# Optimization experiments

Hardware: AMD Instinct MI355X
Metric: run time of the kernel (lower is better)

Reference implementation:

```python
import jax, jax.numpy as jnp
import numpy as np

EPS = 1e-5

def layer_norm(x, g, b):
    m = x.mean(-1, keepdims=True)
    v = ((x - m) ** 2).mean(-1, keepdims=True)
    return (x - m) * jax.lax.rsqrt(v + EPS) * g + b

def setup_inputs() -> dict:
    key = jax.random.key(0)
    ks = jax.random.split(key, 12)
    H = 2048; E = 2048; I = 2048; N = 32
    A = (H + E) // 2  # attention hidden = 2048
    s = lambda fan: 1.0 / np.sqrt(fan)
    inp = {
        "input":   jax.random.normal(ks[0], (I,), jnp.float32),
        "hiddens": jax.random.normal(ks[1], (N, H), jnp.float32),
        "cells":   jax.random.normal(ks[2], (N, H), jnp.float32),
        "external":jax.random.normal(ks[3], (E,), jnp.float32),
        # weights (torch nn.Linear layout: [out, in]); LN enabled -> no biases on linears
        "W_ai":   jax.random.uniform(ks[4], (A, H + E), jnp.float32, -s(H+E), s(H+E)),
        "W_attn": jax.random.uniform(ks[5], (1, A), jnp.float32, -s(A), s(A)),
        "W_merge":jax.random.uniform(ks[6], (H, H), jnp.float32, -s(H), s(H)),
        "W_iou":  jax.random.uniform(ks[7], (3 * H, I + H), jnp.float32, -s(I+H), s(I+H)),
        "W_fi":   jax.random.uniform(ks[8], (H, I), jnp.float32, -s(I), s(I)),
        "W_fh":   jax.random.uniform(ks[9], (H, H), jnp.float32, -s(H), s(H)),
        "g_merge": jnp.ones((H,), jnp.float32), "b_merge": jnp.zeros((H,), jnp.float32),
        "g_f": jnp.ones((H,), jnp.float32), "b_f": jnp.zeros((H,), jnp.float32),
        "g_i": jnp.ones((H,), jnp.float32), "b_i": jnp.zeros((H,), jnp.float32),
        "g_o": jnp.ones((H,), jnp.float32), "b_o": jnp.zeros((H,), jnp.float32),
        "g_u": jnp.ones((H,), jnp.float32), "b_u": jnp.zeros((H,), jnp.float32),
        "g_c": jnp.ones((H,), jnp.float32), "b_c": jnp.zeros((H,), jnp.float32),
    }
    return inp

def reference(input, hiddens, cells, external,
              W_ai, W_attn, W_merge, W_iou, W_fi, W_fh,
              g_merge, b_merge, g_f, b_f, g_i, b_i, g_o, b_o, g_u, b_u, g_c, b_c):
    N, H = hiddens.shape
    # forget-gate preactivations: [H] + [N,H] -> [N,H]
    f_lin = input @ W_fi.T + hiddens @ W_fh.T
    # attentive merge over children
    ext = jnp.broadcast_to(external, (N, external.shape[0]))
    ai = jnp.tanh(jnp.concatenate([hiddens, ext], axis=1) @ W_ai.T)       # [N, (H+E)//2]
    attn = jax.nn.softmax(ai @ W_attn.T, axis=0)                          # [N, 1]
    merged = (hiddens * attn).sum(0)                                      # [H]
    merge_hidden = jnp.tanh(layer_norm(merged @ W_merge.T, g_merge, b_merge))
    # i/o/u gates from [input ; merged_hidden]
    iou = jnp.concatenate([input, merge_hidden]) @ W_iou.T                # [3H]
    i_l, o_l, u_l = jnp.split(iou, 3)
    f = jax.nn.sigmoid(layer_norm(f_lin, g_f, b_f))                       # [N,H]
    i = jax.nn.sigmoid(layer_norm(i_l, g_i, b_i))
    o = jax.nn.sigmoid(layer_norm(o_l, g_o, b_o))
    u = jnp.tanh(layer_norm(u_l, g_u, b_u))                               # dropout=0 -> identity
    new_cell = layer_norm(i * u + (f * cells).sum(0), g_c, b_c)           # [H]
    new_h = o * jnp.tanh(new_cell)
    return new_h, new_cell
```

## Files before the change

kernel.cpp:

```cpp
#include <hip/hip_runtime.h>
#include <hip/hip_bf16.h>

typedef __bf16 bf16_t;
typedef __attribute__((ext_vector_type(8))) __bf16 bf16x8;
typedef __attribute__((ext_vector_type(4))) float f32x4;

#define EPSF 1e-5f

__global__ __launch_bounds__(256) void s1_mega(
    const float* __restrict__ hiddens, const float* __restrict__ external,
    const float* __restrict__ input,
    const float* __restrict__ W_ai, const float* __restrict__ W_fh,
    const float* __restrict__ W_fi, const float* __restrict__ W_attn,
    float* __restrict__ lp, float* __restrict__ fh_out, float* __restrict__ fi_out)
{
    __shared__ float red[4][2][16][16];
    __shared__ float ejs[4][16];

    int b    = blockIdx.x;
    int tid  = threadIdx.x;
    int wave = tid >> 6;
    int lane = tid & 63;

    if (b < 256) {
        bool is_ai = (b < 128);
        int  jt    = is_ai ? b : b - 128;
        int  l15   = lane & 15;
        int  quad  = lane >> 4;
        int  k0    = wave * 512;
        int  wstride = is_ai ? 4096 : 2048;
        const float* W = is_ai ? W_ai : W_fh;

        const float* a0p = hiddens + (size_t)l15 * 2048 + quad * 8 + k0;
        const float* a1p = hiddens + (size_t)(16 + l15) * 2048 + quad * 8 + k0;
        const float* bp  = W + (size_t)(jt * 16 + l15) * wstride + quad * 8 + k0;

        f32x4 acc0 = {0.f, 0.f, 0.f, 0.f};
        f32x4 acc1 = {0.f, 0.f, 0.f, 0.f};
        float ejacc = 0.f;

        if (is_ai) {
            const float* ep = bp + 2048;
            const float* xp = external + quad * 8 + k0;
            #pragma unroll 2
            for (int k = 0; k < 512; k += 32) {
                float4 p0 = *(const float4*)(a0p + k);
                float4 p1 = *(const float4*)(a0p + k + 4);
                float4 q0 = *(const float4*)(a1p + k);
                float4 q1 = *(const float4*)(a1p + k + 4);
                float4 b0 = *(const float4*)(bp + k);
                float4 b1 = *(const float4*)(bp + k + 4);
                float4 e0 = *(const float4*)(ep + k);
                float4 e1 = *(const float4*)(ep + k + 4);
                float4 x0 = *(const float4*)(xp + k);
                float4 x1 = *(const float4*)(xp + k + 4);
                bf16x8 av0, av1, bv;
                av0[0]=(bf16_t)p0.x; av0[1]=(bf16_t)p0.y; av0[2]=(bf16_t)p0.z; av0[3]=(bf16_t)p0.w;
                av0[4]=(bf16_t)p1.x; av0[5]=(bf16_t)p1.y; av0[6]=(bf16_t)p1.z; av0[7]=(bf16_t)p1.w;
                av1[0]=(bf16_t)q0.x; av1[1]=(bf16_t)q0.y; av1[2]=(bf16_t)q0.z; av1[3]=(bf16_t)q0.w;
                av1[4]=(bf16_t)q1.x; av1[5]=(bf16_t)q1.y; av1[6]=(bf16_t)q1.z; av1[7]=(bf16_t)q1.w;
                bv[0]=(bf16_t)b0.x; bv[1]=(bf16_t)b0.y; bv[2]=(bf16_t)b0.z; bv[3]=(bf16_t)b0.w;
                bv[4]=(bf16_t)b1.x; bv[5]=(bf16_t)b1.y; bv[6]=(bf16_t)b1.z; bv[7]=(bf16_t)b1.w;
                acc0 = __builtin_amdgcn_mfma_f32_16x16x32_bf16(av0, bv, acc0, 0, 0, 0);
                acc1 = __builtin_amdgcn_mfma_f32_16x16x32_bf16(av1, bv, acc1, 0, 0, 0);
                ejacc += e0.x*x0.x + e0.y*x0.y + e0.z*x0.z + e0.w*x0.w
                       + e1.x*x1.x + e1.y*x1.y + e1.z*x1.z + e1.w*x1.w;
            }
            ejacc += __shfl_xor(ejacc, 16, 64);
            ejacc += __shfl_xor(ejacc, 32, 64);
            if (quad == 0) ejs[wave][l15] = ejacc;
        } else {
            #pragma unroll 2
            for (int k = 0; k < 512; k += 32) {
                float4 p0 = *(const float4*)(a0p + k);
                float4 p1 = *(const float4*)(a0p + k + 4);
                float4 q0 = *(const float4*)(a1p + k);
                float4 q1 = *(const float4*)(a1p + k + 4);
                float4 b0 = *(const float4*)(bp + k);
                float4 b1 = *(const float4*)(bp + k + 4);
                bf16x8 av0, av1, bv;
                av0[0]=(bf16_t)p0.x; av0[1]=(bf16_t)p0.y; av0[2]=(bf16_t)p0.z; av0[3]=(bf16_t)p0.w;
                av0[4]=(bf16_t)p1.x; av0[5]=(bf16_t)p1.y; av0[6]=(bf16_t)p1.z; av0[7]=(bf16_t)p1.w;
                av1[0]=(bf16_t)q0.x; av1[1]=(bf16_t)q0.y; av1[2]=(bf16_t)q0.z; av1[3]=(bf16_t)q0.w;
                av1[4]=(bf16_t)q1.x; av1[5]=(bf16_t)q1.y; av1[6]=(bf16_t)q1.z; av1[7]=(bf16_t)q1.w;
                bv[0]=(bf16_t)b0.x; bv[1]=(bf16_t)b0.y; bv[2]=(bf16_t)b0.z; bv[3]=(bf16_t)b0.w;
                bv[4]=(bf16_t)b1.x; bv[5]=(bf16_t)b1.y; bv[6]=(bf16_t)b1.z; bv[7]=(bf16_t)b1.w;
                acc0 = __builtin_amdgcn_mfma_f32_16x16x32_bf16(av0, bv, acc0, 0, 0, 0);
                acc1 = __builtin_amdgcn_mfma_f32_16x16x32_bf16(av1, bv, acc1, 0, 0, 0);
            }
        }

        #pragma unroll
        for (int r = 0; r < 4; ++r) {
            red[wave][0][quad * 4 + r][l15] = acc0[r];
            red[wave][1][quad * 4 + r][l15] = acc1[r];
        }
        __syncthreads();

        int row = tid >> 4, col = tid & 15;
        #pragma unroll
        for (int nt = 0; nt < 2; ++nt) {
            float s = red[0][nt][row][col] + red[1][nt][row][col]
                    + red[2][nt][row][col] + red[3][nt][row][col];
            if (is_ai) {
                float ej = ejs[0][col] + ejs[1][col] + ejs[2][col] + ejs[3][col];
                float lg = tanhf(s + ej) * W_attn[jt * 16 + col];
                lg += __shfl_xor(lg, 1, 64);
                lg += __shfl_xor(lg, 2, 64);
                lg += __shfl_xor(lg, 4, 64);
                lg += __shfl_xor(lg, 8, 64);
                if (col == 0) lp[jt * 32 + nt * 16 + row] = lg;
            } else {
                fh_out[(size_t)(nt * 16 + row) * 2048 + jt * 16 + col] = s;
            }
        }
    } else {
        int nb = b - 256;
        int base, nr;
        if (nb < 128) { base = nb * 4;              nr = 1; }
        else          { base = 512 + (nb - 128) * 12; nr = 3; }
        for (int r = 0; r < nr; ++r) {
            int row = base + wave * nr + r;
            const float4* wp = (const float4*)(W_fi + (size_t)row * 2048) + lane;
            const float4* xp = (const float4*)input + lane;
            float acc2 = 0.f;
            #pragma unroll
            for (int k = 0; k < 512; k += 64) {
                float4 w = wp[k];
                float4 v = xp[k];
                acc2 += w.x*v.x + w.y*v.y + w.z*v.z + w.w*v.w;
            }
            #pragma unroll
            for (int off = 32; off; off >>= 1) acc2 += __shfl_down(acc2, off, 64);
            if (lane == 0) fi_out[row] = acc2;
        }
    }
}

__global__ __launch_bounds__(256) void s2_mega(
    const float* __restrict__ fi, const float* __restrict__ fh,
    const float* __restrict__ lp, const float* __restrict__ hiddens,
    float* __restrict__ frs, float* __restrict__ merged)
{
    __shared__ float s1[256], s2[256];
    int b = blockIdx.x, t = threadIdx.x;

    if (b < 32) {
        int n = b;
        float sum = 0.f, sq = 0.f;
        #pragma unroll
        for (int i = 0; i < 8; ++i) {
            int h = t * 8 + i;
            float v = fi[h] + fh[n * 2048 + h];
            sum += v; sq += v * v;
        }
        s1[t] = sum; s2[t] = sq;
        __syncthreads();
        for (int off = 128; off; off >>= 1) {
            if (t < off) { s1[t] += s1[t + off]; s2[t] += s2[t + off]; }
            __syncthreads();
        }
        if (t == 0) {
            const float inv = 1.f / 2048.f;
            float mean = s1[0] * inv;
            frs[n * 2]     = mean;
            frs[n * 2 + 1] = rsqrtf(s2[0] * inv - mean * mean + EPSF);
        }
    } else {
        __shared__ float lred[32][8];
        __shared__ float attnw[32];
        int n = t >> 3, sl = t & 7;
        float p = 0.f;
        #pragma unroll
        for (int m = 0; m < 16; ++m) p += lp[(sl * 16 + m) * 32 + n];
        lred[n][sl] = p;
        __syncthreads();
        if (sl == 0) {
            float lg = 0.f;
            #pragma unroll
            for (int m = 0; m < 8; ++m) lg += lred[n][m];
            lred[n][0] = lg;
        }
        __syncthreads();
        if (t < 32) {
            float mx = -1e30f;
            for (int m = 0; m < 32; ++m) mx = fmaxf(mx, lred[m][0]);
            float ssum = 0.f;
            for (int m = 0; m < 32; ++m) ssum += expf(lred[m][0] - mx);
            attnw[t] = expf(lred[t][0] - mx) / ssum;
        }
        __syncthreads();
        int h = (b - 32) * 256 + t;
        float acc = 0.f;
        #pragma unroll 8
        for (int n2 = 0; n2 < 32; ++n2) acc += attnw[n2] * hiddens[n2 * 2048 + h];
        merged[h] = acc;
    }
}

__global__ __launch_bounds__(256) void s3_mega(
    const float* __restrict__ W_merge, const float* __restrict__ merged,
    const float* __restrict__ fi, const float* __restrict__ fh,
    const float* __restrict__ frs, const float* __restrict__ gf,
    const float* __restrict__ bf_, const float* __restrict__ cells,
    float* __restrict__ mm, float* __restrict__ fc)
{
    int b = blockIdx.x, t = threadIdx.x;
    if (b < 512) {
        int row  = b * 4 + (t >> 6);
        int lane = t & 63;
        const float4* wp = (const float4*)(W_merge + (size_t)row * 2048) + lane;
        const float4* xp = (const float4*)merged + lane;
        float acc = 0.f;
        #pragma unroll
        for (int k = 0; k < 512; k += 64) {
            float4 w = wp[k];
            float4 v = xp[k];
            acc += w.x*v.x + w.y*v.y + w.z*v.z + w.w*v.w;
        }
        #pragma unroll
        for (int off = 32; off; off >>= 1) acc += __shfl_down(acc, off, 64);
        if (lane == 0) mm[row] = acc;
    } else {
        int h = (b - 512) * 256 + t;
        float g = gf[h], bb = bf_[h], f_i = fi[h];
        float acc = 0.f;
        for (int n = 0; n < 32; ++n) {
            float v = (f_i + fh[n * 2048 + h] - frs[n * 2]) * frs[n * 2 + 1] * g + bb;
            float f = 1.f / (1.f + expf(-v));
            acc += f * cells[n * 2048 + h];
        }
        fc[h] = acc;
    }
}

__global__ __launch_bounds__(256, 3) void s4_iou(
    const float* __restrict__ W_iou, const float* __restrict__ mm,
    const float* __restrict__ input, const float* __restrict__ g,
    const float* __restrict__ bvec, float* __restrict__ iou)
{
    int b = blockIdx.x, t = threadIdx.x;
    int wave = t >> 6, lane = t & 63;

    const float4* mm4 = (const float4*)mm;
    const float4* in4 = (const float4*)input;
    const float4* g4  = (const float4*)g;
    const float4* b4  = (const float4*)bvec;

    float4 mv[8];
    #pragma unroll
    for (int k = 0; k < 8; ++k) mv[k] = mm4[lane + 64 * k];
    float sum = 0.f, sq = 0.f;
    #pragma unroll
    for (int k = 0; k < 8; ++k) {
        sum += mv[k].x + mv[k].y + mv[k].z + mv[k].w;
        sq  += mv[k].x*mv[k].x + mv[k].y*mv[k].y + mv[k].z*mv[k].z + mv[k].w*mv[k].w;
    }
    #pragma unroll
    for (int off = 1; off < 64; off <<= 1) {
        sum += __shfl_xor(sum, off, 64);
        sq  += __shfl_xor(sq,  off, 64);
    }
    const float inv = 1.f / 2048.f;
    float mean = sum * inv;
    float r = rsqrtf(sq * inv - mean * mean + EPSF);

    float4 xr[16];
    #pragma unroll
    for (int k = 0; k < 8; ++k) xr[k] = in4[lane + 64 * k];
    #pragma unroll
    for (int k = 0; k < 8; ++k) {
        float4 gv = g4[lane + 64 * k];
        float4 bv = b4[lane + 64 * k];
        xr[8 + k].x = tanhf((mv[k].x - mean) * r * gv.x + bv.x);
        xr[8 + k].y = tanhf((mv[k].y - mean) * r * gv.y + bv.y);
        xr[8 + k].z = tanhf((mv[k].z - mean) * r * gv.z + bv.z);
        xr[8 + k].w = tanhf((mv[k].w - mean) * r * gv.w + bv.w);
    }

    int row0 = (b * 4 + wave) * 2;
    for (int rr = 0; rr < 2; ++rr) {
        const float4* wp = (const float4*)(W_iou + (size_t)(row0 + rr) * 4096);
        float acc = 0.f;
        #pragma unroll
        for (int k = 0; k < 16; ++k) {
            float4 w = wp[lane + 64 * k];
            acc += w.x*xr[k].x + w.y*xr[k].y + w.z*xr[k].z + w.w*xr[k].w;
        }
        #pragma unroll
        for (int off = 32; off; off >>= 1) acc += __shfl_down(acc, off, 64);
        if (lane == 0) iou[row0 + rr] = acc;
    }
}

__global__ __launch_bounds__(256) void s5_tail(
    const float* __restrict__ iou, const float* __restrict__ fc,
    const float* __restrict__ gi, const float* __restrict__ bi,
    const float* __restrict__ go, const float* __restrict__ bo,
    const float* __restrict__ gu, const float* __restrict__ bu,
    const float* __restrict__ gc, const float* __restrict__ bc,
    float* __restrict__ out)
{
    __shared__ float sA[6][256];
    int t = threadIdx.x;
    float vi[8], vo[8], vu[8];
    float si = 0, qi = 0, so = 0, qo = 0, su = 0, qu = 0;
    #pragma unroll
    for (int i = 0; i < 8; ++i) {
        int h = t * 8 + i;
        vi[i] = iou[h]; vo[i] = iou[2048 + h]; vu[i] = iou[4096 + h];
        si += vi[i]; qi += vi[i] * vi[i];
        so += vo[i]; qo += vo[i] * vo[i];
        su += vu[i]; qu += vu[i] * vu[i];
    }
    sA[0][t] = si; sA[1][t] = qi; sA[2][t] = so;
    sA[3][t] = qo; sA[4][t] = su; sA[5][t] = qu;
    __syncthreads();
    for (int off = 128; off; off >>= 1) {
        if (t < off) {
            #pragma unroll
            for (int c = 0; c < 6; ++c) sA[c][t] += sA[c][t + off];
        }
        __syncthreads();
    }
    const float inv = 1.f / 2048.f;
    float mi = sA[0][0] * inv, ri = rsqrtf(sA[1][0] * inv - mi * mi + EPSF);
    float mo = sA[2][0] * inv, ro = rsqrtf(sA[3][0] * inv - mo * mo + EPSF);
    float mu = sA[4][0] * inv, ru = rsqrtf(sA[5][0] * inv - mu * mu + EPSF);
    __syncthreads();

    float o_[8], v_[8];
    float sv = 0, qv = 0;
    #pragma unroll
    for (int i = 0; i < 8; ++i) {
        int h = t * 8 + i;
        float ivl = 1.f / (1.f + expf(-((vi[i] - mi) * ri * gi[h] + bi[h])));
        o_[i]     = 1.f / (1.f + expf(-((vo[i] - mo) * ro * go[h] + bo[h])));
        float uvl = tanhf((vu[i] - mu) * ru * gu[h] + bu[h]);
        v_[i] = ivl * uvl + fc[h];
        sv += v_[i]; qv += v_[i] * v_[i];
    }
    sA[0][t] = sv; sA[1][t] = qv;
    __syncthreads();
    for (int off = 128; off; off >>= 1) {
        if (t < off) { sA[0][t] += sA[0][t + off]; sA[1][t] += sA[1][t + off]; }
        __syncthreads();
    }
    float mc = sA[0][0] * inv, rc = rsqrtf(sA[1][0] * inv - mc * mc + EPSF);
    #pragma unroll
    for (int i = 0; i < 8; ++i) {
        int h = t * 8 + i;
        float nc = (v_[i] - mc) * rc * gc[h] + bc[h];
        float nh = o_[i] * tanhf(nc);
        out[h]        = nh;
        out[2048 + h] = nc;
    }
}

extern "C" void kernel_launch(void* const* d_in, const int* in_sizes, int n_in,
                              void* d_out, int out_size, void* d_ws, size_t ws_size,
                              hipStream_t stream)
{
    const float* input    = (const float*)d_in[0];
    const float* hiddens  = (const float*)d_in[1];
    const float* cells    = (const float*)d_in[2];
    const float* external = (const float*)d_in[3];
    const float* W_ai     = (const float*)d_in[4];
    const float* W_attn   = (const float*)d_in[5];
    const float* W_merge  = (const float*)d_in[6];
    const float* W_iou    = (const float*)d_in[7];
    const float* W_fi     = (const float*)d_in[8];
    const float* W_fh     = (const float*)d_in[9];
    const float* g_merge  = (const float*)d_in[10];
    const float* b_merge  = (const float*)d_in[11];
    const float* g_f      = (const float*)d_in[12];
    const float* b_f      = (const float*)d_in[13];
    const float* g_i      = (const float*)d_in[14];
    const float* b_i      = (const float*)d_in[15];
    const float* g_o      = (const float*)d_in[16];
    const float* b_o      = (const float*)d_in[17];
    const float* g_u      = (const float*)d_in[18];
    const float* b_u      = (const float*)d_in[19];
    const float* g_c      = (const float*)d_in[20];
    const float* b_c      = (const float*)d_in[21];

    float* ws = (float*)d_ws;
    float* ws_fh     = ws;
    float* ws_fi     = ws + 65536;
    float* ws_lp     = ws + 67584;
    float* ws_frs    = ws + 71680;
    float* ws_merged = ws + 71744;
    float* ws_mm     = ws + 73792;
    float* ws_fc     = ws + 75840;
    float* ws_iou    = ws + 77888;
    float* out = (float*)d_out;

    s1_mega<<<512, 256, 0, stream>>>(hiddens, external, input,
                                     W_ai, W_fh, W_fi, W_attn,
                                     ws_lp, ws_fh, ws_fi);
    s2_mega<<<40, 256, 0, stream>>>(ws_fi, ws_fh, ws_lp, hiddens,
                                    ws_frs, ws_merged);
    s3_mega<<<520, 256, 0, stream>>>(W_merge, ws_merged, ws_fi, ws_fh,
                                     ws_frs, g_f, b_f, cells, ws_mm, ws_fc);
    s4_iou<<<768, 256, 0, stream>>>(W_iou, ws_mm, input, g_merge, b_merge, ws_iou);
    s5_tail<<<1, 256, 0, stream>>>(ws_iou, ws_fc, g_i, b_i, g_o, b_o,
                                   g_u, b_u, g_c, b_c, out);
}
```

Measured before the change: 281.4 us.

## Fuse five stage kernels into one persistent kernel with grid barriers

Replaces the five kernel launches with a single 256-block persistent kernel that separates the stages with atomic-counter grid barriers. The input half of the W_iou GEMV is moved into stage 1 so it can run early, and stage 4 accumulates the merged-hidden half into the same buffer. This targets the launch gaps and tail idling between dependent small stages. In exchange it depends on all 256 blocks being co-resident, adds a memset and spin-wait cost, and removes the unroll pragmas from the MFMA loops.

```diff
diff --git a/kernel.cpp b/kernel.cpp
--- a/kernel.cpp
+++ b/kernel.cpp
@@ -6,23 +6,49 @@
 typedef __attribute__((ext_vector_type(4))) float f32x4;
 
 #define EPSF 1e-5f
-
-__global__ __launch_bounds__(256) void s1_mega(
-    const float* __restrict__ hiddens, const float* __restrict__ external,
-    const float* __restrict__ input,
-    const float* __restrict__ W_ai, const float* __restrict__ W_fh,
-    const float* __restrict__ W_fi, const float* __restrict__ W_attn,
-    float* __restrict__ lp, float* __restrict__ fh_out, float* __restrict__ fi_out)
+#define NB 256
+
+__device__ __forceinline__ void gbar(int* cnt, int target) {
+    __syncthreads();
+    if (threadIdx.x == 0) {
+        __hip_atomic_fetch_add(cnt, 1, __ATOMIC_ACQ_REL, __HIP_MEMORY_SCOPE_AGENT);
+        while (__hip_atomic_load(cnt, __ATOMIC_ACQUIRE, __HIP_MEMORY_SCOPE_AGENT) < target)
+            __builtin_amdgcn_s_sleep(2);
+    }
+    __syncthreads();
+}
+
+__global__ __launch_bounds__(256, 2) void fused_cell(
+    const float* __restrict__ input, const float* __restrict__ hiddens,
+    const float* __restrict__ cells, const float* __restrict__ external,
+    const float* __restrict__ W_ai, const float* __restrict__ W_attn,
+    const float* __restrict__ W_merge, const float* __restrict__ W_iou,
+    const float* __restrict__ W_fi, const float* __restrict__ W_fh,
+    const float* __restrict__ g_merge, const float* __restrict__ b_merge,
+    const float* __restrict__ g_f, const float* __restrict__ b_f,
+    const float* __restrict__ gi, const float* __restrict__ bi,
+    const float* __restrict__ go, const float* __restrict__ bo,
+    const float* __restrict__ gu, const float* __restrict__ bu,
+    const float* __restrict__ gc, const float* __restrict__ bc,
+    float* __restrict__ ws_fh, float* __restrict__ ws_fi,
+    float* __restrict__ ws_lp, float* __restrict__ ws_frs,
+    float* __restrict__ ws_merged, float* __restrict__ ws_mm,
+    float* __restrict__ ws_fc, float* __restrict__ ws_iou,
+    int* __restrict__ bar, float* __restrict__ out)
 {
     __shared__ float red[4][2][16][16];
     __shared__ float ejs[4][16];
+    __shared__ float sb1[256], sb2[256];
+    __shared__ float lred[32][8];
+    __shared__ float attnw[32];
+    __shared__ float sA6[6][256];
 
     int b    = blockIdx.x;
     int tid  = threadIdx.x;
     int wave = tid >> 6;
     int lane = tid & 63;
 
-    if (b < 256) {
+    {
         bool is_ai = (b < 128);
         int  jt    = is_ai ? b : b - 128;
         int  l15   = lane & 15;
@@ -42,7 +68,6 @@
         if (is_ai) {
             const float* ep = bp + 2048;
             const float* xp = external + quad * 8 + k0;
-            #pragma unroll 2
             for (int k = 0; k < 512; k += 32) {
                 float4 p0 = *(const float4*)(a0p + k);
                 float4 p1 = *(const float4*)(a0p + k + 4);
@@ -70,7 +95,6 @@
             ejacc += __shfl_xor(ejacc, 32, 64);
             if (quad == 0) ejs[wave][l15] = ejacc;
         } else {
-            #pragma unroll 2
             for (int k = 0; k < 512; k += 32) {
                 float4 p0 = *(const float4*)(a0p + k);
                 float4 p1 = *(const float4*)(a0p + k + 4);
@@ -109,70 +133,68 @@
                 lg += __shfl_xor(lg, 2, 64);
                 lg += __shfl_xor(lg, 4, 64);
                 lg += __shfl_xor(lg, 8, 64);
-                if (col == 0) lp[jt * 32 + nt * 16 + row] = lg;
+                if (col == 0) ws_lp[jt * 32 + nt * 16 + row] = lg;
             } else {
-                fh_out[(size_t)(nt * 16 + row) * 2048 + jt * 16 + col] = s;
-            }
-        }
-    } else {
-        int nb = b - 256;
-        int base, nr;
-        if (nb < 128) { base = nb * 4;              nr = 1; }
-        else          { base = 512 + (nb - 128) * 12; nr = 3; }
-        for (int r = 0; r < nr; ++r) {
-            int row = base + wave * nr + r;
-            const float4* wp = (const float4*)(W_fi + (size_t)row * 2048) + lane;
-            const float4* xp = (const float4*)input + lane;
-            float acc2 = 0.f;
-            #pragma unroll
-            for (int k = 0; k < 512; k += 64) {
-                float4 w = wp[k];
-                float4 v = xp[k];
-                acc2 += w.x*v.x + w.y*v.y + w.z*v.z + w.w*v.w;
-            }
-            #pragma unroll
-            for (int off = 32; off; off >>= 1) acc2 += __shfl_down(acc2, off, 64);
-            if (lane == 0) fi_out[row] = acc2;
-        }
-    }
-}
-
-__global__ __launch_bounds__(256) void s2_mega(
-    const float* __restrict__ fi, const float* __restrict__ fh,
-    const float* __restrict__ lp, const float* __restrict__ hiddens,
-    float* __restrict__ frs, float* __restrict__ merged)
-{
-    __shared__ float s1[256], s2[256];
-    int b = blockIdx.x, t = threadIdx.x;
+                ws_fh[(size_t)(nt * 16 + row) * 2048 + jt * 16 + col] = s;
+            }
+        }
+
+        const float4* in4 = (const float4*)input;
+        float4 xr[8];
+        #pragma unroll
+        for (int k = 0; k < 8; ++k) xr[k] = in4[lane + 64 * k];
+
+        int base  = is_ai ? jt * 24 : 3072 + jt * 40;
+        int nrows = is_ai ? 6 : 10;
+        int r0 = base + wave * nrows;
+        for (int i = 0; i < nrows; ++i) {
+            int r = r0 + i;
+            const float4* wp = (r < 2048)
+                ? (const float4*)(W_fi + (size_t)r * 2048)
+                : (const float4*)(W_iou + (size_t)(r - 2048) * 4096);
+            float acc = 0.f;
+            #pragma unroll
+            for (int k = 0; k < 8; ++k) {
+                float4 w = wp[lane + 64 * k];
+                acc += w.x*xr[k].x + w.y*xr[k].y + w.z*xr[k].z + w.w*xr[k].w;
+            }
+            #pragma unroll
+            for (int off = 32; off; off >>= 1) acc += __shfl_down(acc, off, 64);
+            if (lane == 0) {
+                if (r < 2048) ws_fi[r] = acc;
+                else          ws_iou[r - 2048] = acc;
+            }
+        }
+    }
+
+    gbar(bar, NB);
 
     if (b < 32) {
         int n = b;
         float sum = 0.f, sq = 0.f;
         #pragma unroll
         for (int i = 0; i < 8; ++i) {
-            int h = t * 8 + i;
-            float v = fi[h] + fh[n * 2048 + h];
+            int h = tid * 8 + i;
+            float v = ws_fi[h] + ws_fh[n * 2048 + h];
             sum += v; sq += v * v;
         }
-        s1[t] = sum; s2[t] = sq;
+        sb1[tid] = sum; sb2[tid] = sq;
         __syncthreads();
         for (int off = 128; off; off >>= 1) {
-            if (t < off) { s1[t] += s1[t + off]; s2[t] += s2[t + off]; }
+            if (tid < off) { sb1[tid] += sb1[tid + off]; sb2[tid] += sb2[tid + off]; }
             __syncthreads();
         }
-        if (t == 0) {
+        if (tid == 0) {
             const float inv = 1.f / 2048.f;
-            float mean = s1[0] * inv;
-            frs[n * 2]     = mean;
-            frs[n * 2 + 1] = rsqrtf(s2[0] * inv - mean * mean + EPSF);
-        }
-    } else {
-        __shared__ float lred[32][8];
-        __shared__ float attnw[32];
-        int n = t >> 3, sl = t & 7;
+            float mean = sb1[0] * inv;
+            ws_frs[n * 2]     = mean;
+            ws_frs[n * 2 + 1] = rsqrtf(sb2[0] * inv - mean * mean + EPSF);
+        }
+    } else if (b < 40) {
+        int n = tid >> 3, sl = tid & 7;
         float p = 0.f;
         #pragma unroll
-        for (int m = 0; m < 16; ++m) p += lp[(sl * 16 + m) * 32 + n];
+        for (int m = 0; m < 16; ++m) p += ws_lp[(sl * 16 + m) * 32 + n];
         lred[n][sl] = p;
         __syncthreads();
         if (sl == 0) {
@@ -182,178 +204,162 @@
             lred[n][0] = lg;
         }
         __syncthreads();
-        if (t < 32) {
+        if (tid < 32) {
             float mx = -1e30f;
             for (int m = 0; m < 32; ++m) mx = fmaxf(mx, lred[m][0]);
             float ssum = 0.f;
             for (int m = 0; m < 32; ++m) ssum += expf(lred[m][0] - mx);
-            attnw[t] = expf(lred[t][0] - mx) / ssum;
-        }
-        __syncthreads();
-        int h = (b - 32) * 256 + t;
+            attnw[tid] = expf(lred[tid][0] - mx) / ssum;
+        }
+        __syncthreads();
+        int h = (b - 32) * 256 + tid;
         float acc = 0.f;
         #pragma unroll 8
         for (int n2 = 0; n2 < 32; ++n2) acc += attnw[n2] * hiddens[n2 * 2048 + h];
-        merged[h] = acc;
-    }
-}
-
-__global__ __launch_bounds__(256) void s3_mega(
-    const float* __restrict__ W_merge, const float* __restrict__ merged,
-    const float* __restrict__ fi, const float* __restrict__ fh,
-    const float* __restrict__ frs, const float* __restrict__ gf,
-    const float* __restrict__ bf_, const float* __restrict__ cells,
-    float* __restrict__ mm, float* __restrict__ fc)
-{
-    int b = blockIdx.x, t = threadIdx.x;
-    if (b < 512) {
-        int row  = b * 4 + (t >> 6);
-        int lane = t & 63;
-        const float4* wp = (const float4*)(W_merge + (size_t)row * 2048) + lane;
-        const float4* xp = (const float4*)merged + lane;
-        float acc = 0.f;
-        #pragma unroll
-        for (int k = 0; k < 512; k += 64) {
-            float4 w = wp[k];
-            float4 v = xp[k];
-            acc += w.x*v.x + w.y*v.y + w.z*v.z + w.w*v.w;
-        }
-        #pragma unroll
-        for (int off = 32; off; off >>= 1) acc += __shfl_down(acc, off, 64);
-        if (lane == 0) mm[row] = acc;
-    } else {
-        int h = (b - 512) * 256 + t;
-        float g = gf[h], bb = bf_[h], f_i = fi[h];
-        float acc = 0.f;
-        for (int n = 0; n < 32; ++n) {
-            float v = (f_i + fh[n * 2048 + h] - frs[n * 2]) * frs[n * 2 + 1] * g + bb;
-            float f = 1.f / (1.f + expf(-v));
-            acc += f * cells[n * 2048 + h];
-        }
-        fc[h] = acc;
-    }
-}
-
-__global__ __launch_bounds__(256, 3) void s4_iou(
-    const float* __restrict__ W_iou, const float* __restrict__ mm,
-    const float* __restrict__ input, const float* __restrict__ g,
-    const float* __restrict__ bvec, float* __restrict__ iou)
-{
-    int b = blockIdx.x, t = threadIdx.x;
-    int wave = t >> 6, lane = t & 63;
-
-    const float4* mm4 = (const float4*)mm;
-    const float4* in4 = (const float4*)input;
-    const float4* g4  = (const float4*)g;
-    const float4* b4  = (const float4*)bvec;
-
-    float4 mv[8];
-    #pragma unroll
-    for (int k = 0; k < 8; ++k) mv[k] = mm4[lane + 64 * k];
-    float sum = 0.f, sq = 0.f;
-    #pragma unroll
-    for (int k = 0; k < 8; ++k) {
-        sum += mv[k].x + mv[k].y + mv[k].z + mv[k].w;
-        sq  += mv[k].x*mv[k].x + mv[k].y*mv[k].y + mv[k].z*mv[k].z + mv[k].w*mv[k].w;
-    }
-    #pragma unroll
-    for (int off = 1; off < 64; off <<= 1) {
-        sum += __shfl_xor(sum, off, 64);
-        sq  += __shfl_xor(sq,  off, 64);
-    }
-    const float inv = 1.f / 2048.f;
-    float mean = sum * inv;
-    float r = rsqrtf(sq * inv - mean * mean + EPSF);
-
-    float4 xr[16];
-    #pragma unroll
-    for (int k = 0; k < 8; ++k) xr[k] = in4[lane + 64 * k];
-    #pragma unroll
-    for (int k = 0; k < 8; ++k) {
-        float4 gv = g4[lane + 64 * k];
-        float4 bv = b4[lane + 64 * k];
-        xr[8 + k].x = tanhf((mv[k].x - mean) * r * gv.x + bv.x);
-        xr[8 + k].y = tanhf((mv[k].y - mean) * r * gv.y + bv.y);
-        xr[8 + k].z = tanhf((mv[k].z - mean) * r * gv.z + bv.z);
-        xr[8 + k].w = tanhf((mv[k].w - mean) * r * gv.w + bv.w);
-    }
-
-    int row0 = (b * 4 + wave) * 2;
-    for (int rr = 0; rr < 2; ++rr) {
-        const float4* wp = (const float4*)(W_iou + (size_t)(row0 + rr) * 4096);
-        float acc = 0.f;
-        #pragma unroll
-        for (int k = 0; k < 16; ++k) {
-            float4 w = wp[lane + 64 * k];
-            acc += w.x*xr[k].x + w.y*xr[k].y + w.z*xr[k].z + w.w*xr[k].w;
-        }
-        #pragma unroll
-        for (int off = 32; off; off >>= 1) acc += __shfl_down(acc, off, 64);
-        if (lane == 0) iou[row0 + rr] = acc;
-    }
-}
-
-__global__ __launch_bounds__(256) void s5_tail(
-    const float* __restrict__ iou, const float* __restrict__ fc,
-    const float* __restrict__ gi, const float* __restrict__ bi,
-    const float* __restrict__ go, const float* __restrict__ bo,
-    const float* __restrict__ gu, const float* __restrict__ bu,
-    const float* __restrict__ gc, const float* __restrict__ bc,
-    float* __restrict__ out)
-{
-    __shared__ float sA[6][256];
-    int t = threadIdx.x;
-    float vi[8], vo[8], vu[8];
-    float si = 0, qi = 0, so = 0, qo = 0, su = 0, qu = 0;
-    #pragma unroll
-    for (int i = 0; i < 8; ++i) {
-        int h = t * 8 + i;
-        vi[i] = iou[h]; vo[i] = iou[2048 + h]; vu[i] = iou[4096 + h];
-        si += vi[i]; qi += vi[i] * vi[i];
-        so += vo[i]; qo += vo[i] * vo[i];
-        su += vu[i]; qu += vu[i] * vu[i];
-    }
-    sA[0][t] = si; sA[1][t] = qi; sA[2][t] = so;
-    sA[3][t] = qo; sA[4][t] = su; sA[5][t] = qu;
-    __syncthreads();
-    for (int off = 128; off; off >>= 1) {
-        if (t < off) {
-            #pragma unroll
-            for (int c = 0; c < 6; ++c) sA[c][t] += sA[c][t + off];
-        }
-        __syncthreads();
-    }
-    const float inv = 1.f / 2048.f;
-    float mi = sA[0][0] * inv, ri = rsqrtf(sA[1][0] * inv - mi * mi + EPSF);
-    float mo = sA[2][0] * inv, ro = rsqrtf(sA[3][0] * inv - mo * mo + EPSF);
-    float mu = sA[4][0] * inv, ru = rsqrtf(sA[5][0] * inv - mu * mu + EPSF);
-    __syncthreads();
-
-    float o_[8], v_[8];
-    float sv = 0, qv = 0;
-    #pragma unroll
-    for (int i = 0; i < 8; ++i) {
-        int h = t * 8 + i;
-        float ivl = 1.f / (1.f + expf(-((vi[i] - mi) * ri * gi[h] + bi[h])));
-        o_[i]     = 1.f / (1.f + expf(-((vo[i] - mo) * ro * go[h] + bo[h])));
-        float uvl = tanhf((vu[i] - mu) * ru * gu[h] + bu[h]);
-        v_[i] = ivl * uvl + fc[h];
-        sv += v_[i]; qv += v_[i] * v_[i];
-    }
-    sA[0][t] = sv; sA[1][t] = qv;
-    __syncthreads();
-    for (int off = 128; off; off >>= 1) {
-        if (t < off) { sA[0][t] += sA[0][t + off]; sA[1][t] += sA[1][t + off]; }
-        __syncthreads();
-    }
-    float mc = sA[0][0] * inv, rc = rsqrtf(sA[1][0] * inv - mc * mc + EPSF);
-    #pragma unroll
-    for (int i = 0; i < 8; ++i) {
-        int h = t * 8 + i;
-        float nc = (v_[i] - mc) * rc * gc[h] + bc[h];
-        float nh = o_[i] * tanhf(nc);
-        out[h]        = nh;
-        out[2048 + h] = nc;
+        ws_merged[h] = acc;
+    }
+
+    gbar(bar, 2 * NB);
+
+    {
+        const float4* xp = (const float4*)ws_merged;
+        int rowc = b * 8 + wave * 2;
+        for (int rr = 0; rr < 2; ++rr) {
+            int row = rowc + rr;
+            const float4* wp = (const float4*)(W_merge + (size_t)row * 2048);
+            float acc = 0.f;
+            #pragma unroll
+            for (int k = 0; k < 8; ++k) {
+                float4 w = wp[lane + 64 * k];
+                float4 v = xp[lane + 64 * k];
+                acc += w.x*v.x + w.y*v.y + w.z*v.z + w.w*v.w;
+            }
+            #pragma unroll
+            for (int off = 32; off; off >>= 1) acc += __shfl_down(acc, off, 64);
+            if (lane == 0) ws_mm[row] = acc;
+        }
+        if (b < 8) {
+            int h = b * 256 + tid;
+            float g = g_f[h], bb = b_f[h], f_i = ws_fi[h];
+            float acc = 0.f;
+            for (int n = 0; n < 32; ++n) {
+                float v = (f_i + ws_fh[n * 2048 + h] - ws_frs[n * 2]) * ws_frs[n * 2 + 1] * g + bb;
+                float f = 1.f / (1.f + expf(-v));
+                acc += f * cells[n * 2048 + h];
+            }
+            ws_fc[h] = acc;
+        }
+    }
+
+    gbar(bar, 3 * NB);
+
+    {
+        const float4* mm4 = (const float4*)ws_mm;
+        const float4* g4  = (const float4*)g_merge;
+        const float4* b4  = (const float4*)b_merge;
+
+        float4 mv[8];
+        #pragma unroll
+        for (int k = 0; k < 8; ++k) mv[k] = mm4[lane + 64 * k];
+        float sum = 0.f, sq = 0.f;
+        #pragma unroll
+        for (int k = 0; k < 8; ++k) {
+            sum += mv[k].x + mv[k].y + mv[k].z + mv[k].w;
+            sq  += mv[k].x*mv[k].x + mv[k].y*mv[k].y + mv[k].z*mv[k].z + mv[k].w*mv[k].w;
+        }
+        #pragma unroll
+        for (int off = 1; off < 64; off <<= 1) {
+            sum += __shfl_xor(sum, off, 64);
+            sq  += __shfl_xor(sq,  off, 64);
+        }
+        const float inv = 1.f / 2048.f;
+        float mean = sum * inv;
+        float r = rsqrtf(sq * inv - mean * mean + EPSF);
+
+        float4 mh[8];
+        #pragma unroll
+        for (int k = 0; k < 8; ++k) {
+            float4 gv = g4[lane + 64 * k];
+            float4 bv = b4[lane + 64 * k];
+            mh[k].x = tanhf((mv[k].x - mean) * r * gv.x + bv.x);
+            mh[k].y = tanhf((mv[k].y - mean) * r * gv.y + bv.y);
+            mh[k].z = tanhf((mv[k].z - mean) * r * gv.z + bv.z);
+            mh[k].w = tanhf((mv[k].w - mean) * r * gv.w + bv.w);
+        }
+
+        int r0 = b * 24 + wave * 6;
+        for (int i = 0; i < 6; ++i) {
+            int row = r0 + i;
+            const float4* wp = (const float4*)(W_iou + (size_t)row * 4096 + 2048);
+            float acc = 0.f;
+            #pragma unroll
+            for (int k = 0; k < 8; ++k) {
+                float4 w = wp[lane + 64 * k];
+                acc += w.x*mh[k].x + w.y*mh[k].y + w.z*mh[k].z + w.w*mh[k].w;
+            }
+            #pragma unroll
+            for (int off = 32; off; off >>= 1) acc += __shfl_down(acc, off, 64);
+            if (lane == 0) ws_iou[row] += acc;
+        }
+    }
+
+    gbar(bar, 4 * NB);
+
+    if (b != 0) return;
+    {
+        int t = tid;
+        float vi[8], vo[8], vu[8];
+        float si = 0, qi = 0, so = 0, qo = 0, su = 0, qu = 0;
+        #pragma unroll
+        for (int i = 0; i < 8; ++i) {
+            int h = t * 8 + i;
+            vi[i] = ws_iou[h]; vo[i] = ws_iou[2048 + h]; vu[i] = ws_iou[4096 + h];
+            si += vi[i]; qi += vi[i] * vi[i];
+            so += vo[i]; qo += vo[i] * vo[i];
+            su += vu[i]; qu += vu[i] * vu[i];
+        }
+        sA6[0][t] = si; sA6[1][t] = qi; sA6[2][t] = so;
+        sA6[3][t] = qo; sA6[4][t] = su; sA6[5][t] = qu;
+        __syncthreads();
+        for (int off = 128; off; off >>= 1) {
+            if (t < off) {
+                #pragma unroll
+                for (int c = 0; c < 6; ++c) sA6[c][t] += sA6[c][t + off];
+            }
+            __syncthreads();
+        }
+        const float inv = 1.f / 2048.f;
+        float mi = sA6[0][0] * inv, ri = rsqrtf(sA6[1][0] * inv - mi * mi + EPSF);
+        float mo = sA6[2][0] * inv, ro = rsqrtf(sA6[3][0] * inv - mo * mo + EPSF);
+        float mu = sA6[4][0] * inv, ru = rsqrtf(sA6[5][0] * inv - mu * mu + EPSF);
+        __syncthreads();
+
+        float o_[8], v_[8];
+        float sv = 0, qv = 0;
+        #pragma unroll
+        for (int i = 0; i < 8; ++i) {
+            int h = t * 8 + i;
+            float ivl = 1.f / (1.f + expf(-((vi[i] - mi) * ri * gi[h] + bi[h])));
+            o_[i]     = 1.f / (1.f + expf(-((vo[i] - mo) * ro * go[h] + bo[h])));
+            float uvl = tanhf((vu[i] - mu) * ru * gu[h] + bu[h]);
+            v_[i] = ivl * uvl + ws_fc[h];
+            sv += v_[i]; qv += v_[i] * v_[i];
+        }
+        sA6[0][t] = sv; sA6[1][t] = qv;
+        __syncthreads();
+        for (int off = 128; off; off >>= 1) {
+            if (t < off) { sA6[0][t] += sA6[0][t + off]; sA6[1][t] += sA6[1][t + off]; }
+            __syncthreads();
+        }
+        float mc = sA6[0][0] * inv, rc = rsqrtf(sA6[1][0] * inv - mc * mc + EPSF);
+        #pragma unroll
+        for (int i = 0; i < 8; ++i) {
+            int h = t * 8 + i;
+            float nc = (v_[i] - mc) * rc * gc[h] + bc[h];
+            float nh = o_[i] * tanhf(nc);
+            out[h]        = nh;
+            out[2048 + h] = nc;
+        }
     }
 }
 
@@ -393,16 +399,14 @@
     float* ws_mm     = ws + 73792;
     float* ws_fc     = ws + 75840;
     float* ws_iou    = ws + 77888;
+    int*   ws_bar    = (int*)(ws + 84032);
     float* out = (float*)d_out;
 
-    s1_mega<<<512, 256, 0, stream>>>(hiddens, external, input,
-                                     W_ai, W_fh, W_fi, W_attn,
-                                     ws_lp, ws_fh, ws_fi);
-    s2_mega<<<40, 256, 0, stream>>>(ws_fi, ws_fh, ws_lp, hiddens,
-                                    ws_frs, ws_merged);
-    s3_mega<<<520, 256, 0, stream>>>(W_merge, ws_merged, ws_fi, ws_fh,
-                                     ws_frs, g_f, b_f, cells, ws_mm, ws_fc);
-    s4_iou<<<768, 256, 0, stream>>>(W_iou, ws_mm, input, g_merge, b_merge, ws_iou);
-    s5_tail<<<1, 256, 0, stream>>>(ws_iou, ws_fc, g_i, b_i, g_o, b_o,
-                                   g_u, b_u, g_c, b_c, out);
+    hipMemsetAsync(ws_bar, 0, 64, stream);
+    fused_cell<<<NB, 256, 0, stream>>>(input, hiddens, cells, external,
+                                       W_ai, W_attn, W_merge, W_iou, W_fi, W_fh,
+                                       g_merge, b_merge, g_f, b_f,
+                                       g_i, b_i, g_o, b_o, g_u, b_u, g_c, b_c,
+                                       ws_fh, ws_fi, ws_lp, ws_frs, ws_merged,
+                                       ws_mm, ws_fc, ws_iou, ws_bar, out);
 }
```

New measurement: 359.9 us. +27.9%, slower.

## Hoist input half of W_iou GEMV into first kernel and fuse tail via last-block

Applied to the files above, without the earlier changes.

The half of the iou GEMV that depends only on `input` (W_iou columns 0..2047) moves into the first kernel, where it streams alongside W_fi. Only the merge-dependent half is left on the critical path after W_merge. The separate single-block tail kernel is removed: the iou kernel uses an atomic done counter so the last block runs the final layer norms, saving a launch at the cost of a memset and fence/atomic overhead. Row indexing in k1 now covers 2048 fi rows plus 6144 iou rows over 512 extra blocks, each wave handling 4 rows with two rows loaded at once.

```diff
diff --git a/kernel.cpp b/kernel.cpp
--- a/kernel.cpp
+++ b/kernel.cpp
@@ -7,12 +7,14 @@
 
 #define EPSF 1e-5f
 
-__global__ __launch_bounds__(256) void s1_mega(
+__global__ __launch_bounds__(256, 3) void k1_streams(
     const float* __restrict__ hiddens, const float* __restrict__ external,
     const float* __restrict__ input,
     const float* __restrict__ W_ai, const float* __restrict__ W_fh,
-    const float* __restrict__ W_fi, const float* __restrict__ W_attn,
-    float* __restrict__ lp, float* __restrict__ fh_out, float* __restrict__ fi_out)
+    const float* __restrict__ W_fi, const float* __restrict__ W_iou,
+    const float* __restrict__ W_attn,
+    float* __restrict__ lp, float* __restrict__ fh_out,
+    float* __restrict__ fi_out, float* __restrict__ iou_out)
 {
     __shared__ float red[4][2][16][16];
     __shared__ float ejs[4][16];
@@ -115,29 +117,45 @@
             }
         }
     } else {
-        int nb = b - 256;
-        int base, nr;
-        if (nb < 128) { base = nb * 4;              nr = 1; }
-        else          { base = 512 + (nb - 128) * 12; nr = 3; }
-        for (int r = 0; r < nr; ++r) {
-            int row = base + wave * nr + r;
-            const float4* wp = (const float4*)(W_fi + (size_t)row * 2048) + lane;
-            const float4* xp = (const float4*)input + lane;
-            float acc2 = 0.f;
-            #pragma unroll
-            for (int k = 0; k < 512; k += 64) {
-                float4 w = wp[k];
-                float4 v = xp[k];
-                acc2 += w.x*v.x + w.y*v.y + w.z*v.z + w.w*v.w;
-            }
-            #pragma unroll
-            for (int off = 32; off; off >>= 1) acc2 += __shfl_down(acc2, off, 64);
-            if (lane == 0) fi_out[row] = acc2;
+        const float4* in4 = (const float4*)input;
+        float4 xr[8];
+        #pragma unroll
+        for (int k = 0; k < 8; ++k) xr[k] = in4[lane + 64 * k];
+
+        int r0 = (b - 256) * 16 + wave * 4;
+        #pragma unroll
+        for (int p = 0; p < 2; ++p) {
+            int ra = r0 + p * 2;
+            int rb = ra + 1;
+            const float4* wa = (ra < 2048)
+                ? (const float4*)(W_fi + (size_t)ra * 2048)
+                : (const float4*)(W_iou + (size_t)(ra - 2048) * 4096);
+            const float4* wb = (rb < 2048)
+                ? (const float4*)(W_fi + (size_t)rb * 2048)
+                : (const float4*)(W_iou + (size_t)(rb - 2048) * 4096);
+            float4 A[8], B[8];
+            #pragma unroll
+            for (int k = 0; k < 8; ++k) { A[k] = wa[lane + 64 * k]; B[k] = wb[lane + 64 * k]; }
+            float accA = 0.f, accB = 0.f;
+            #pragma unroll
+            for (int k = 0; k < 8; ++k) {
+                accA += A[k].x*xr[k].x + A[k].y*xr[k].y + A[k].z*xr[k].z + A[k].w*xr[k].w;
+                accB += B[k].x*xr[k].x + B[k].y*xr[k].y + B[k].z*xr[k].z + B[k].w*xr[k].w;
+            }
+            #pragma unroll
+            for (int off = 32; off; off >>= 1) {
+                accA += __shfl_down(accA, off, 64);
+                accB += __shfl_down(accB, off, 64);
+            }
+            if (lane == 0) {
+                if (ra < 2048) fi_out[ra] = accA; else iou_out[ra - 2048] = accA;
+                if (rb < 2048) fi_out[rb] = accB; else iou_out[rb - 2048] = accB;
+            }
         }
     }
 }
 
-__global__ __launch_bounds__(256) void s2_mega(
+__global__ __launch_bounds__(256) void k2_mid(
     const float* __restrict__ fi, const float* __restrict__ fh,
     const float* __restrict__ lp, const float* __restrict__ hiddens,
     float* __restrict__ frs, float* __restrict__ merged)
@@ -198,7 +216,7 @@
     }
 }
 
-__global__ __launch_bounds__(256) void s3_mega(
+__global__ __launch_bounds__(256) void k3_mid(
     const float* __restrict__ W_merge, const float* __restrict__ merged,
     const float* __restrict__ fi, const float* __restrict__ fh,
     const float* __restrict__ frs, const float* __restrict__ gf,
@@ -234,126 +252,135 @@
     }
 }
 
-__global__ __launch_bounds__(256, 3) void s4_iou(
+__global__ __launch_bounds__(256, 2) void k4_tail(
     const float* __restrict__ W_iou, const float* __restrict__ mm,
-    const float* __restrict__ input, const float* __restrict__ g,
-    const float* __restrict__ bvec, float* __restrict__ iou)
-{
-    int b = blockIdx.x, t = threadIdx.x;
-    int wave = t >> 6, lane = t & 63;
-
-    const float4* mm4 = (const float4*)mm;
-    const float4* in4 = (const float4*)input;
-    const float4* g4  = (const float4*)g;
-    const float4* b4  = (const float4*)bvec;
-
-    float4 mv[8];
-    #pragma unroll
-    for (int k = 0; k < 8; ++k) mv[k] = mm4[lane + 64 * k];
-    float sum = 0.f, sq = 0.f;
-    #pragma unroll
-    for (int k = 0; k < 8; ++k) {
-        sum += mv[k].x + mv[k].y + mv[k].z + mv[k].w;
-        sq  += mv[k].x*mv[k].x + mv[k].y*mv[k].y + mv[k].z*mv[k].z + mv[k].w*mv[k].w;
-    }
-    #pragma unroll
-    for (int off = 1; off < 64; off <<= 1) {
-        sum += __shfl_xor(sum, off, 64);
-        sq  += __shfl_xor(sq,  off, 64);
-    }
-    const float inv = 1.f / 2048.f;
-    float mean = sum * inv;
-    float r = rsqrtf(sq * inv - mean * mean + EPSF);
-
-    float4 xr[16];
-    #pragma unroll
-    for (int k = 0; k < 8; ++k) xr[k] = in4[lane + 64 * k];
-    #pragma unroll
-    for (int k = 0; k < 8; ++k) {
-        float4 gv = g4[lane + 64 * k];
-        float4 bv = b4[lane + 64 * k];
-        xr[8 + k].x = tanhf((mv[k].x - mean) * r * gv.x + bv.x);
-        xr[8 + k].y = tanhf((mv[k].y - mean) * r * gv.y + bv.y);
-        xr[8 + k].z = tanhf((mv[k].z - mean) * r * gv.z + bv.z);
-        xr[8 + k].w = tanhf((mv[k].w - mean) * r * gv.w + bv.w);
-    }
-
-    int row0 = (b * 4 + wave) * 2;
-    for (int rr = 0; rr < 2; ++rr) {
-        const float4* wp = (const float4*)(W_iou + (size_t)(row0 + rr) * 4096);
-        float acc = 0.f;
-        #pragma unroll
-        for (int k = 0; k < 16; ++k) {
-            float4 w = wp[lane + 64 * k];
-            acc += w.x*xr[k].x + w.y*xr[k].y + w.z*xr[k].z + w.w*xr[k].w;
-        }
-        #pragma unroll
-        for (int off = 32; off; off >>= 1) acc += __shfl_down(acc, off, 64);
-        if (lane == 0) iou[row0 + rr] = acc;
-    }
-}
-
-__global__ __launch_bounds__(256) void s5_tail(
-    const float* __restrict__ iou, const float* __restrict__ fc,
+    const float* __restrict__ g_merge, const float* __restrict__ b_merge,
+    float* __restrict__ iou, const float* __restrict__ fc,
     const float* __restrict__ gi, const float* __restrict__ bi,
     const float* __restrict__ go, const float* __restrict__ bo,
     const float* __restrict__ gu, const float* __restrict__ bu,
     const float* __restrict__ gc, const float* __restrict__ bc,
-    float* __restrict__ out)
+    int* __restrict__ done, float* __restrict__ out)
 {
-    __shared__ float sA[6][256];
-    int t = threadIdx.x;
-    float vi[8], vo[8], vu[8];
-    float si = 0, qi = 0, so = 0, qo = 0, su = 0, qu = 0;
-    #pragma unroll
-    for (int i = 0; i < 8; ++i) {
-        int h = t * 8 + i;
-        vi[i] = iou[h]; vo[i] = iou[2048 + h]; vu[i] = iou[4096 + h];
-        si += vi[i]; qi += vi[i] * vi[i];
-        so += vo[i]; qo += vo[i] * vo[i];
-        su += vu[i]; qu += vu[i] * vu[i];
-    }
-    sA[0][t] = si; sA[1][t] = qi; sA[2][t] = so;
-    sA[3][t] = qo; sA[4][t] = su; sA[5][t] = qu;
+    __shared__ int is_last;
+    __shared__ float sA6[6][256];
+    int b = blockIdx.x, tid = threadIdx.x;
+    int wave = tid >> 6, lane = tid & 63;
+
+    {
+        const float4* mm4 = (const float4*)mm;
+        const float4* g4  = (const float4*)g_merge;
+        const float4* b4  = (const float4*)b_merge;
+
+        float4 mv[8];
+        #pragma unroll
+        for (int k = 0; k < 8; ++k) mv[k] = mm4[lane + 64 * k];
+        float sum = 0.f, sq = 0.f;
+        #pragma unroll
+        for (int k = 0; k < 8; ++k) {
+            sum += mv[k].x + mv[k].y + mv[k].z + mv[k].w;
+            sq  += mv[k].x*mv[k].x + mv[k].y*mv[k].y + mv[k].z*mv[k].z + mv[k].w*mv[k].w;
+        }
+        #pragma unroll
+        for (int off = 1; off < 64; off <<= 1) {
+            sum += __shfl_xor(sum, off, 64);
+            sq  += __shfl_xor(sq,  off, 64);
+        }
+        const float inv = 1.f / 2048.f;
+        float mean = sum * inv;
+        float r = rsqrtf(sq * inv - mean * mean + EPSF);
+
+        float4 mh[8];
+        #pragma unroll
+        for (int k = 0; k < 8; ++k) {
+            float4 gv = g4[lane + 64 * k];
+            float4 bv = b4[lane + 64 * k];
+            mh[k].x = tanhf((mv[k].x - mean) * r * gv.x + bv.x);
+            mh[k].y = tanhf((mv[k].y - mean) * r * gv.y + bv.y);
+            mh[k].z = tanhf((mv[k].z - mean) * r * gv.z + bv.z);
+            mh[k].w = tanhf((mv[k].w - mean) * r * gv.w + bv.w);
+        }
+
+        int r0 = b * 12 + wave * 3;
+        for (int i = 0; i < 3; ++i) {
+            int row = r0 + i;
+            const float4* wp = (const float4*)(W_iou + (size_t)row * 4096 + 2048);
+            float acc = 0.f;
+            #pragma unroll
+            for (int k = 0; k < 8; ++k) {
+                float4 w = wp[lane + 64 * k];
+                acc += w.x*mh[k].x + w.y*mh[k].y + w.z*mh[k].z + w.w*mh[k].w;
+            }
+            #pragma unroll
+            for (int off = 32; off; off >>= 1) acc += __shfl_down(acc, off, 64);
+            if (lane == 0) iou[row] += acc;
+        }
+    }
+
+    __threadfence();
     __syncthreads();
-    for (int off = 128; off; off >>= 1) {
-        if (t < off) {
-            #pragma unroll
-            for (int c = 0; c < 6; ++c) sA[c][t] += sA[c][t + off];
-        }
-        __syncthreads();
-    }
-    const float inv = 1.f / 2048.f;
-    float mi = sA[0][0] * inv, ri = rsqrtf(sA[1][0] * inv - mi * mi + EPSF);
-    float mo = sA[2][0] * inv, ro = rsqrtf(sA[3][0] * inv - mo * mo + EPSF);
-    float mu = sA[4][0] * inv, ru = rsqrtf(sA[5][0] * inv - mu * mu + EPSF);
+    if (tid == 0) {
+        int old = __hip_atomic_fetch_add(done, 1, __ATOMIC_ACQ_REL, __HIP_MEMORY_SCOPE_AGENT);
+        is_last = (old == (int)gridDim.x - 1);
+    }
     __syncthreads();
-
-    float o_[8], v_[8];
-    float sv = 0, qv = 0;
-    #pragma unroll
-    for (int i = 0; i < 8; ++i) {
-        int h = t * 8 + i;
-        float ivl = 1.f / (1.f + expf(-((vi[i] - mi) * ri * gi[h] + bi[h])));
-        o_[i]     = 1.f / (1.f + expf(-((vo[i] - mo) * ro * go[h] + bo[h])));
-        float uvl = tanhf((vu[i] - mu) * ru * gu[h] + bu[h]);
-        v_[i] = ivl * uvl + fc[h];
-        sv += v_[i]; qv += v_[i] * v_[i];
-    }
-    sA[0][t] = sv; sA[1][t] = qv;
-    __syncthreads();
-    for (int off = 128; off; off >>= 1) {
-        if (t < off) { sA[0][t] += sA[0][t + off]; sA[1][t] += sA[1][t + off]; }
-        __syncthreads();
-    }
-    float mc = sA[0][0] * inv, rc = rsqrtf(sA[1][0] * inv - mc * mc + EPSF);
-    #pragma unroll
-    for (int i = 0; i < 8; ++i) {
-        int h = t * 8 + i;
-        float nc = (v_[i] - mc) * rc * gc[h] + bc[h];
-        float nh = o_[i] * tanhf(nc);
-        out[h]        = nh;
-        out[2048 + h] = nc;
+    if (!is_last) return;
+    __threadfence();
+
+    {
+        int t = tid;
+        float vi[8], vo[8], vu[8];
+        float si = 0, qi = 0, so = 0, qo = 0, su = 0, qu = 0;
+        #pragma unroll
+        for (int i = 0; i < 8; ++i) {
+            int h = t * 8 + i;
+            vi[i] = iou[h]; vo[i] = iou[2048 + h]; vu[i] = iou[4096 + h];
+            si += vi[i]; qi += vi[i] * vi[i];
+            so += vo[i]; qo += vo[i] * vo[i];
+            su += vu[i]; qu += vu[i] * vu[i];
+        }
+        sA6[0][t] = si; sA6[1][t] = qi; sA6[2][t] = so;
+        sA6[3][t] = qo; sA6[4][t] = su; sA6[5][t] = qu;
+        __syncthreads();
+        for (int off = 128; off; off >>= 1) {
+            if (t < off) {
+                #pragma unroll
+                for (int c = 0; c < 6; ++c) sA6[c][t] += sA6[c][t + off];
+            }
+            __syncthreads();
+        }
+        const float inv = 1.f / 2048.f;
+        float mi = sA6[0][0] * inv, ri = rsqrtf(sA6[1][0] * inv - mi * mi + EPSF);
+        float mo = sA6[2][0] * inv, ro = rsqrtf(sA6[3][0] * inv - mo * mo + EPSF);
+        float mu = sA6[4][0] * inv, ru = rsqrtf(sA6[5][0] * inv - mu * mu + EPSF);
+        __syncthreads();
+
+        float o_[8], v_[8];
+        float sv = 0, qv = 0;
+        #pragma unroll
+        for (int i = 0; i < 8; ++i) {
+            int h = t * 8 + i;
+            float ivl = 1.f / (1.f + expf(-((vi[i] - mi) * ri * gi[h] + bi[h])));
+            o_[i]     = 1.f / (1.f + expf(-((vo[i] - mo) * ro * go[h] + bo[h])));
+            float uvl = tanhf((vu[i] - mu) * ru * gu[h] + bu[h]);
+            v_[i] = ivl * uvl + fc[h];
+            sv += v_[i]; qv += v_[i] * v_[i];
+        }
+        sA6[0][t] = sv; sA6[1][t] = qv;
+        __syncthreads();
+        for (int off = 128; off; off >>= 1) {
+            if (t < off) { sA6[0][t] += sA6[0][t + off]; sA6[1][t] += sA6[1][t + off]; }
+            __syncthreads();
+        }
+        float mc = sA6[0][0] * inv, rc = rsqrtf(sA6[1][0] * inv - mc * mc + EPSF);
+        #pragma unroll
+        for (int i = 0; i < 8; ++i) {
+            int h = t * 8 + i;
+            float nc = (v_[i] - mc) * rc * gc[h] + bc[h];
+            float nh = o_[i] * tanhf(nc);
+            out[h]        = nh;
+            out[2048 + h] = nc;
+        }
     }
 }
 
@@ -393,16 +420,18 @@
     float* ws_mm     = ws + 73792;
     float* ws_fc     = ws + 75840;
     float* ws_iou    = ws + 77888;
+    int*   ws_done   = (int*)(ws + 84032);
     float* out = (float*)d_out;
 
-    s1_mega<<<512, 256, 0, stream>>>(hiddens, external, input,
-                                     W_ai, W_fh, W_fi, W_attn,
-                                     ws_lp, ws_fh, ws_fi);
-    s2_mega<<<40, 256, 0, stream>>>(ws_fi, ws_fh, ws_lp, hiddens,
-                                    ws_frs, ws_merged);
-    s3_mega<<<520, 256, 0, stream>>>(W_merge, ws_merged, ws_fi, ws_fh,
-                                     ws_frs, g_f, b_f, cells, ws_mm, ws_fc);
-    s4_iou<<<768, 256, 0, stream>>>(W_iou, ws_mm, input, g_merge, b_merge, ws_iou);
-    s5_tail<<<1, 256, 0, stream>>>(ws_iou, ws_fc, g_i, b_i, g_o, b_o,
-                                   g_u, b_u, g_c, b_c, out);
+    hipMemsetAsync(ws_done, 0, 64, stream);
+    k1_streams<<<768, 256, 0, stream>>>(hiddens, external, input,
+                                        W_ai, W_fh, W_fi, W_iou, W_attn,
+                                        ws_lp, ws_fh, ws_fi, ws_iou);
+    k2_mid<<<40, 256, 0, stream>>>(ws_fi, ws_fh, ws_lp, hiddens,
+                                   ws_frs, ws_merged);
+    k3_mid<<<520, 256, 0, stream>>>(W_merge, ws_merged, ws_fi, ws_fh,
+                                    ws_frs, g_f, b_f, cells, ws_mm, ws_fc);
+    k4_tail<<<512, 256, 0, stream>>>(W_iou, ws_mm, g_merge, b_merge,
+                                     ws_iou, ws_fc, g_i, b_i, g_o, b_o,
+                                     g_u, b_u, g_c, b_c, ws_done, out);
 }
```

Result: slower. 354.0 us (+25.8%).
